# Optimization experiments

Hardware: AMD Instinct MI355X
Metric: run time of the kernel (lower is better)

Reference implementation:

```python
import jax, jax.numpy as jnp
import numpy as np

B, D, U = 64, 256, 256

def setup_inputs() -> dict:
    key = jax.random.key(0)
    ks = jax.random.split(key, 16)
    init_mu = 0.05
    inputs = jax.random.normal(ks[0], (B, D), jnp.float32)
    prev_state = 0.1 * jax.random.normal(ks[1], (B, U), jnp.float32)
    A = jax.random.normal(ks[2], (B, U, U), jnp.float32)
    # symmetric, diagonally boosted covariance-like state
    Sigma_state = 0.01 * (A + jnp.swapaxes(A, 1, 2)) + 0.1 * jnp.eye(U, dtype=jnp.float32)
    def w(k, shape):
        return init_mu * jax.random.normal(k, shape, jnp.float32)
    def s(k):
        return jax.random.uniform(k, (U,), jnp.float32, -4.5, -2.2)
    return {
        'inputs': inputs, 'prev_state': prev_state, 'Sigma_state': Sigma_state,
        'U_z': w(ks[3], (D, U)), 'uz_sigma': s(ks[4]), 'W_z': w(ks[5], (U, U)), 'wz_sigma': s(ks[6]),
        'U_r': w(ks[7], (D, U)), 'ur_sigma': s(ks[8]), 'W_r': w(ks[9], (U, U)), 'wr_sigma': s(ks[10]),
        'U_h': w(ks[11], (D, U)), 'uh_sigma': s(ks[12]), 'W_h': w(ks[13], (U, U)), 'wh_sigma': s(ks[14]),
    }

def _outer(a, b):  # [B,u],[B,u] -> [B,u,u]
    return a[:, :, None] * b[:, None, :]

def _quad(W, S):  # W^T @ S @ W, S is [B,u,u]
    return jnp.matmul(jnp.matmul(W.T, S), W)

def _x_sigma_w(x, sv):  # ||x||^2 * diag(softplus sigma)
    return jnp.sum(x * x, axis=1)[:, None, None] * jnp.diag(sv)

def _tr_sigma_w(S, sv):  # trace(S) * diag(softplus sigma)
    return jnp.trace(S, axis1=1, axis2=2)[:, None, None] * jnp.diag(sv)

def _hadamard_sigma(S1, S2, m1, m2):
    # S1*S2 + diag(m1) S2 diag(m1) + diag(m2) S1 diag(m2) as elementwise/broadcast
    return S1 * S2 + _outer(m1, m1) * S2 + _outer(m2, m2) * S1

def reference(inputs, prev_state, Sigma_state, U_z, uz_sigma, W_z, wz_sigma,
              U_r, ur_sigma, W_r, wr_sigma, U_h, uh_sigma, W_h, wh_sigma):
    sp = jax.nn.softplus
    # --- z gate ---
    az = inputs @ U_z + prev_state @ W_z
    z = jax.nn.sigmoid(az)
    gz = z * (1.0 - z)  # d sigmoid
    Sz = (_quad(W_z, Sigma_state) + _x_sigma_w(prev_state, sp(wz_sigma))
          + _tr_sigma_w(Sigma_state, sp(wz_sigma)) + _x_sigma_w(inputs, sp(uz_sigma)))
    Sigma_out_z = Sz * _outer(gz, gz)
    # --- r gate ---
    ar = inputs @ U_r + prev_state @ W_r
    r = jax.nn.sigmoid(ar)
    gr = r * (1.0 - r)
    Sr = (_quad(W_r, Sigma_state) + _x_sigma_w(prev_state, sp(wr_sigma))
          + _tr_sigma_w(Sigma_state, sp(wr_sigma)) + _x_sigma_w(inputs, sp(ur_sigma)))
    Sigma_out_r = Sr * _outer(gr, gr)
    # --- h candidate ---
    g_in = prev_state * r
    ah = inputs @ U_h + g_in @ W_h
    h = jnp.tanh(ah)
    gh = 1.0 - h * h  # d tanh
    sigma_g = _hadamard_sigma(Sigma_state, Sigma_out_r, prev_state, r)
    Sh = (_quad(W_h, sigma_g) + _x_sigma_w(g_in, sp(wh_sigma))
          + _tr_sigma_w(sigma_g, sp(wh_sigma)) + _x_sigma_w(inputs, sp(uh_sigma)))
    Sigma_out_h = Sh * _outer(gh, gh)
    # --- output combination ---
    mu_out = z * prev_state + (1.0 - z) * h
    sigma_a = _hadamard_sigma(Sigma_out_z, Sigma_state, z, prev_state)
    sigma_b = _hadamard_sigma(Sigma_out_z, Sigma_out_h, 1.0 - z, h)
    Sigma_out = (sigma_a + sigma_b
                 - Sigma_out_z * _outer(prev_state, h)
                 - Sigma_out_z * _outer(h, prev_state))
    Sigma_out = jnp.where(jnp.isnan(Sigma_out) | jnp.isinf(Sigma_out),
                          jnp.zeros_like(Sigma_out), Sigma_out)
    eye = jnp.eye(Sigma_out.shape[-1], dtype=Sigma_out.dtype)
    d = jnp.abs(jnp.diagonal(Sigma_out, axis1=1, axis2=2))
    Sigma_out = Sigma_out * (1.0 - eye) + d[:, :, None] * eye
    return mu_out, Sigma_out
```

## Files before the change

kernel.cpp:

```cpp
#include <hip/hip_runtime.h>
#include <math.h>

#define UDIM 256
#define BATCH 64
#define MATN 65536
#define PITCH 280

typedef __bf16 bf16x8 __attribute__((ext_vector_type(8)));
typedef float  f32x4  __attribute__((ext_vector_type(4)));

__device__ __forceinline__ float softplusf(float x) { return log1pf(expf(x)); }
__device__ __forceinline__ float sigmoidf_(float x) { return 1.f/(1.f+expf(-x)); }

__device__ __forceinline__ bf16x8 frag_load(const __bf16* base, int rt, int kt, int lane) {
  return *(const bf16x8*)(base + (((size_t)(rt*8 + kt))*64 + lane)*8);
}

__device__ __forceinline__ bf16x8 cvt8(const float* p) {
  const float4 f0 = *(const float4*)p;
  const float4 f1 = *(const float4*)(p + 4);
  bf16x8 v;
  v[0]=(__bf16)f0.x; v[1]=(__bf16)f0.y; v[2]=(__bf16)f0.z; v[3]=(__bf16)f0.w;
  v[4]=(__bf16)f1.x; v[5]=(__bf16)f1.y; v[6]=(__bf16)f1.z; v[7]=(__bf16)f1.w;
  return v;
}

__global__ __launch_bounds__(256) void prep6(
    const float* __restrict__ Uz, const float* __restrict__ Wz,
    const float* __restrict__ Ur, const float* __restrict__ Wr,
    const float* __restrict__ Uh, const float* __restrict__ Wh,
    __bf16* __restrict__ Fu_z, __bf16* __restrict__ Fw_z,
    __bf16* __restrict__ Fu_r, __bf16* __restrict__ Fw_r,
    __bf16* __restrict__ Fu_h, __bf16* __restrict__ Fw_h,
    const float* __restrict__ S, const float* __restrict__ x,
    const float* __restrict__ prev, float* __restrict__ scal)
{
  const int t = threadIdx.x;
  if (blockIdx.z == 6) {
    const int blk = blockIdx.y*4 + blockIdx.x;
    const int b = blk*4 + (t >> 6), l = t & 63;
    const float4 xv = *(const float4*)(x + b*UDIM + l*4);
    float s0 = xv.x*xv.x + xv.y*xv.y + xv.z*xv.z + xv.w*xv.w;
    const float4 pv = *(const float4*)(prev + b*UDIM + l*4);
    float s1 = pv.x*pv.x + pv.y*pv.y + pv.z*pv.z + pv.w*pv.w;
    float s2 = 0.f;
#pragma unroll
    for (int e = 0; e < 4; ++e)
      s2 += S[(size_t)b*MATN + (size_t)(l*4 + e)*257];
    for (int off = 32; off; off >>= 1) {
      s0 += __shfl_down(s0, off);
      s1 += __shfl_down(s1, off);
      s2 += __shfl_down(s2, off);
    }
    if (l == 0) {
      atomicAdd(&scal[b], s0);
      atomicAdd(&scal[64 + b], s1);
      atomicAdd(&scal[128 + b], s2);
    }
    return;
  }
  const float* W; __bf16* F;
  switch (blockIdx.z) {
    case 0: W = Uz; F = Fu_z; break;  case 1: W = Wz; F = Fw_z; break;
    case 2: W = Ur; F = Fu_r; break;  case 3: W = Wr; F = Fw_r; break;
    case 4: W = Uh; F = Fu_h; break;  default: W = Wh; F = Fw_h; break;
  }
  const int k0 = blockIdx.y*64, n0 = blockIdx.x*64;
  __shared__ float tile[64][65];
  const int tx = t & 15, ty = t >> 4;
#pragma unroll
  for (int rr = 0; rr < 4; ++rr) {
    const int row = ty*4 + rr;
    const float4 f = *(const float4*)(W + (size_t)(k0 + row)*UDIM + n0 + tx*4);
    tile[row][tx*4+0] = f.x; tile[row][tx*4+1] = f.y;
    tile[row][tx*4+2] = f.z; tile[row][tx*4+3] = f.w;
  }
  __syncthreads();
#pragma unroll
  for (int ss = 0; ss < 2; ++ss) {
    const int s = t + ss*256;
    const int rt_l = s >> 7, kt_l = (s >> 6) & 1, lane = s & 63;
    const int nl = rt_l*16 + (lane & 15), kb = kt_l*32 + (lane >> 4)*8;
    __align__(16) __bf16 tmp[8];
#pragma unroll
    for (int e = 0; e < 8; ++e) tmp[e] = (__bf16)tile[kb + e][nl];
    *(uint4*)(F + (((size_t)((((n0 >> 4) + rt_l)*8) + (k0 >> 5) + kt_l))*64 + lane)*8)
        = *(const uint4*)tmp;
  }
}

__global__ __launch_bounds__(256) void sconvf(
    const float* __restrict__ S, __bf16* __restrict__ Sf)
{
  const int bx = blockIdx.x, by = blockIdx.y, b = blockIdx.z;
  const size_t sb = (size_t)b * MATN;
  const int t = threadIdx.x;
#pragma unroll
  for (int ss = 0; ss < 2; ++ss) {
    const int s = t + ss*256;
    const int chunk = s >> 6, lane = s & 63;
    const int rt_l = chunk >> 1, kt_l = chunk & 1;
    const int row = by*64 + rt_l*16 + (lane & 15);
    const int col = bx*64 + kt_l*32 + (lane >> 4)*8;
    const bf16x8 v = cvt8(S + sb + (size_t)row*UDIM + col);
    *(bf16x8*)(Sf + sb + (((size_t)((by*4 + rt_l)*8 + bx*2 + kt_l))*64 + lane)*8) = v;
  }
}

__global__ __launch_bounds__(256) void gates_zr(
    const float* __restrict__ x, const float* __restrict__ prev,
    const __bf16* __restrict__ Fu_z, const __bf16* __restrict__ Fw_z,
    const __bf16* __restrict__ Fu_r, const __bf16* __restrict__ Fw_r,
    float* __restrict__ zb, float* __restrict__ rb,
    float* __restrict__ gzb, float* __restrict__ grb,
    float* __restrict__ gin, float* __restrict__ scal)
{
  const int jt = blockIdx.x;
  const int gate = blockIdx.y;
  const __bf16* FU = gate ? Fu_r : Fu_z;
  const __bf16* FW = gate ? Fw_r : Fw_z;
  const int t = threadIdx.x, w = t >> 6, l = t & 63, r = l & 15, q = l >> 4;
  const int mrow = w*16 + r;

  f32x4 acc[4] = {};
#pragma unroll
  for (int ks = 0; ks < 16; ++ks) {
    const int k0 = ks*32;
    const float* asrc; const __bf16* B; int kk;
    if (k0 < 256) { asrc = x    + (size_t)mrow*UDIM + k0         + q*8; B = FU; kk = k0; }
    else          { asrc = prev + (size_t)mrow*UDIM + (k0 - 256) + q*8; B = FW; kk = k0 - 256; }
    const bf16x8 af = cvt8(asrc);
#pragma unroll
    for (int ni = 0; ni < 4; ++ni) {
      const bf16x8 bv = frag_load(B, jt*4 + ni, kk >> 5, l);
      acc[ni] = __builtin_amdgcn_mfma_f32_16x16x32_bf16(af, bv, acc[ni], 0, 0, 0);
    }
  }

  if (gate == 0) {
#pragma unroll
    for (int ni = 0; ni < 4; ++ni) {
      const int n = jt*64 + ni*16 + r;
#pragma unroll
      for (int v = 0; v < 4; ++v) {
        const int m = w*16 + q*4 + v;
        const float zv = sigmoidf_(acc[ni][v]);
        zb[m*UDIM + n]  = zv;
        gzb[m*UDIM + n] = zv * (1.f - zv);
      }
    }
  } else {
    float ggp[4] = {0.f, 0.f, 0.f, 0.f};
#pragma unroll
    for (int ni = 0; ni < 4; ++ni) {
      const int n = jt*64 + ni*16 + r;
#pragma unroll
      for (int v = 0; v < 4; ++v) {
        const int m = w*16 + q*4 + v;
        const float rv = sigmoidf_(acc[ni][v]);
        const float pv = prev[m*UDIM + n];
        const float g2 = pv * rv;
        rb[m*UDIM + n]  = rv;
        grb[m*UDIM + n] = rv * (1.f - rv);
        gin[m*UDIM + n] = g2;
        ggp[v] += g2 * g2;
      }
    }
#pragma unroll
    for (int s = 1; s < 16; s <<= 1)
#pragma unroll
      for (int v = 0; v < 4; ++v) ggp[v] += __shfl_xor(ggp[v], s);
    if (r == 0)
#pragma unroll
      for (int v = 0; v < 4; ++v)
        atomicAdd(&scal[192 + w*16 + q*4 + v], ggp[v]);
  }
}

__global__ __launch_bounds__(256) void gates_h(
    const float* __restrict__ x, const float* __restrict__ gin,
    const __bf16* __restrict__ Fu_h, const __bf16* __restrict__ Fw_h,
    const float* __restrict__ prev, const float* __restrict__ zb,
    float* __restrict__ hb, float* __restrict__ ghb, float* __restrict__ mu_out)
{
  const int jt = blockIdx.x;
  const int t = threadIdx.x, w = t >> 6, l = t & 63, r = l & 15, q = l >> 4;
  const int mrow = w*16 + r;

  f32x4 acc[4] = {};
#pragma unroll
  for (int ks = 0; ks < 16; ++ks) {
    const int k0 = ks*32;
    const float* asrc; const __bf16* B; int kk;
    if (k0 < 256) { asrc = x   + (size_t)mrow*UDIM + k0         + q*8; B = Fu_h; kk = k0; }
    else          { asrc = gin + (size_t)mrow*UDIM + (k0 - 256) + q*8; B = Fw_h; kk = k0 - 256; }
    const bf16x8 af = cvt8(asrc);
#pragma unroll
    for (int ni = 0; ni < 4; ++ni) {
      const bf16x8 bv = frag_load(B, jt*4 + ni, kk >> 5, l);
      acc[ni] = __builtin_amdgcn_mfma_f32_16x16x32_bf16(af, bv, acc[ni], 0, 0, 0);
    }
  }
#pragma unroll
  for (int ni = 0; ni < 4; ++ni) {
    const int n = jt*64 + ni*16 + r;
#pragma unroll
    for (int v = 0; v < 4; ++v) {
      const int m = w*16 + q*4 + v;
      const float hv = tanhf(acc[ni][v]);
      const float zv = zb[m*UDIM + n];
      hb[m*UDIM + n]  = hv;
      ghb[m*UDIM + n] = 1.f - hv*hv;
      mu_out[m*UDIM + n] = zv * prev[m*UDIM + n] + (1.f - zv) * hv;
    }
  }
}

__global__ __launch_bounds__(256, 4) void quad_zr(
    const float* __restrict__ S, const __bf16* __restrict__ Sf,
    const float* __restrict__ prev,
    const float* __restrict__ rb, const float* __restrict__ gzb,
    const float* __restrict__ grb,
    const float* __restrict__ wz_s, const float* __restrict__ uz_s,
    const float* __restrict__ wr_s, const float* __restrict__ ur_s,
    const __bf16* __restrict__ Fw_z, const __bf16* __restrict__ Fw_r,
    float* __restrict__ scal, __bf16* __restrict__ Szb, __bf16* __restrict__ G)
{
  const int bid = blockIdx.x;
  const int s = bid >> 6, b = bid & 63;
  const size_t sb = (size_t)b * MATN;
  const int t = threadIdx.x, w = t >> 6, l = t & 63, r = l & 15, q = l >> 4;
  const __bf16* Sfb = Sf + sb;

  __shared__ __align__(16) __bf16 Tz[16*PITCH];
  __shared__ __align__(16) __bf16 Tr[16*PITCH];

  f32x4 az[4] = {}, ar[4] = {};
#pragma unroll
  for (int kt = 0; kt < 8; ++kt) {
    const bf16x8 afz = frag_load(Fw_z, s, kt, l);
    const bf16x8 afr = frag_load(Fw_r, s, kt, l);
#pragma unroll
    for (int ct = 0; ct < 4; ++ct) {
      const bf16x8 bv = frag_load(Sfb, w*4 + ct, kt, l);
      az[ct] = __builtin_amdgcn_mfma_f32_16x16x32_bf16(afz, bv, az[ct], 0, 0, 0);
      ar[ct] = __builtin_amdgcn_mfma_f32_16x16x32_bf16(afr, bv, ar[ct], 0, 0, 0);
    }
  }
#pragma unroll
  for (int ct = 0; ct < 4; ++ct)
#pragma unroll
    for (int v = 0; v < 4; ++v) {
      const int row = q*4 + v, col = w*64 + ct*16 + r;
      Tz[row*PITCH + col] = (__bf16)az[ct][v];
      Tr[row*PITCH + col] = (__bf16)ar[ct][v];
    }
  __syncthreads();

  f32x4 qz[4] = {}, qr[4] = {};
#pragma unroll
  for (int kt = 0; kt < 8; ++kt) {
    const bf16x8 atz = *(const bf16x8*)&Tz[r*PITCH + kt*32 + q*8];
    const bf16x8 atr = *(const bf16x8*)&Tr[r*PITCH + kt*32 + q*8];
#pragma unroll
    for (int ct = 0; ct < 4; ++ct) {
      const bf16x8 bz = frag_load(Fw_z, w*4 + ct, kt, l);
      const bf16x8 br = frag_load(Fw_r, w*4 + ct, kt, l);
      qz[ct] = __builtin_amdgcn_mfma_f32_16x16x32_bf16(atz, bz, qz[ct], 0, 0, 0);
      qr[ct] = __builtin_amdgcn_mfma_f32_16x16x32_bf16(atr, br, qr[ct], 0, 0, 0);
    }
  }

  const float xx = scal[b];
  const float dscal = scal[64 + b] + scal[128 + b];
  const int ib = s*16 + q*4;

  {
    const f32x4 g4 = *(const f32x4*)(gzb + b*UDIM + ib);
    __align__(16) __bf16 o16[16];
#pragma unroll
    for (int ct = 0; ct < 4; ++ct) {
      const int j = (w*4 + ct)*16 + r;
      const float gj = gzb[b*UDIM + j];
#pragma unroll
      for (int v = 0; v < 4; ++v) {
        const int i = ib + v;
        float qv = qz[ct][v];
        if (i == j) qv += dscal*softplusf(wz_s[i]) + xx*softplusf(uz_s[i]);
        o16[ct*4 + v] = (__bf16)(qv * g4[v] * gj);
      }
    }
    __bf16* dst = Szb + ((size_t)(b*16 + s)*256 + t)*16;
    *(uint4*)dst       = *(const uint4*)&o16[0];
    *(uint4*)(dst + 8) = *(const uint4*)&o16[8];
  }

  float gvals[16];
  float trg = 0.f;
  {
    const f32x4 g4 = *(const f32x4*)(grb + b*UDIM + ib);
    const f32x4 p4 = *(const f32x4*)(prev + b*UDIM + ib);
    const f32x4 r4 = *(const f32x4*)(rb + b*UDIM + ib);
#pragma unroll
    for (int ct = 0; ct < 4; ++ct) {
      const int j = (w*4 + ct)*16 + r;
      const float gj = grb[b*UDIM + j];
      const float pj = prev[b*UDIM + j];
      const float rj = rb[b*UDIM + j];
#pragma unroll
      for (int v = 0; v < 4; ++v) {
        const int i = ib + v;
        float qv = qr[ct][v];
        if (i == j) qv += dscal*softplusf(wr_s[i]) + xx*softplusf(ur_s[i]);
        const float Sg = qv * g4[v] * gj;
        const float sv = S[sb + (size_t)i*UDIM + j];
        const float go = Sg*(sv + p4[v]*pj) + r4[v]*rj*sv;
        gvals[ct*4 + v] = go;
        if (i == j) trg += go;
      }
    }
  }
  if (trg != 0.f) atomicAdd(&scal[256 + b], trg);

  __syncthreads();
#pragma unroll
  for (int ct = 0; ct < 4; ++ct)
#pragma unroll
    for (int v = 0; v < 4; ++v)
      Tz[(q*4 + v)*PITCH + w*64 + ct*16 + r] = (__bf16)gvals[ct*4 + v];
  __syncthreads();
#pragma unroll
  for (int ee = 0; ee < 2; ++ee) {
    const int e = t + ee*256;
    const int kt = e >> 6, le = e & 63;
    const uint4 vv = *(const uint4*)&Tz[(le & 15)*PITCH + kt*32 + (le >> 4)*8];
    *(uint4*)(G + sb + (((size_t)(s*8 + kt))*64 + le)*8) = vv;
  }
}

__global__ __launch_bounds__(256, 4) void quad_h(
    const float* __restrict__ S, const __bf16* __restrict__ Szb,
    const float* __restrict__ prev, const float* __restrict__ zb,
    const float* __restrict__ hb, const float* __restrict__ ghb,
    const float* __restrict__ wh_s, const float* __restrict__ uh_s,
    const __bf16* __restrict__ Fw_h, const __bf16* __restrict__ G,
    const float* __restrict__ scal, float* __restrict__ out_sig)
{
  const int bid = blockIdx.x;
  const int s = bid >> 6, b = bid & 63;
  const size_t sb = (size_t)b * MATN;
  const int t = threadIdx.x, w = t >> 6, l = t & 63, r = l & 15, q = l >> 4;
  const __bf16* Gb = G + sb;

  __shared__ __align__(16) __bf16 Th[16*PITCH];

  f32x4 ah[4] = {};
#pragma unroll
  for (int kt = 0; kt < 8; ++kt) {
    const bf16x8 af = frag_load(Fw_h, s, kt, l);
#pragma unroll
    for (int ct = 0; ct < 4; ++ct) {
      const bf16x8 bv = frag_load(Gb, w*4 + ct, kt, l);
      ah[ct] = __builtin_amdgcn_mfma_f32_16x16x32_bf16(af, bv, ah[ct], 0, 0, 0);
    }
  }
#pragma unroll
  for (int ct = 0; ct < 4; ++ct)
#pragma unroll
    for (int v = 0; v < 4; ++v)
      Th[(q*4 + v)*PITCH + w*64 + ct*16 + r] = (__bf16)ah[ct][v];
  __syncthreads();

  f32x4 qh[4] = {};
#pragma unroll
  for (int kt = 0; kt < 8; ++kt) {
    const bf16x8 at = *(const bf16x8*)&Th[r*PITCH + kt*32 + q*8];
#pragma unroll
    for (int ct = 0; ct < 4; ++ct) {
      const bf16x8 bv = frag_load(Fw_h, w*4 + ct, kt, l);
      qh[ct] = __builtin_amdgcn_mfma_f32_16x16x32_bf16(at, bv, qh[ct], 0, 0, 0);
    }
  }

  const float xx = scal[b];
  const float dscal = scal[192 + b] + scal[256 + b];
  const int ib = s*16 + q*4;

  const __bf16* szp = Szb + ((size_t)(b*16 + s)*256 + t)*16;
  __align__(16) __bf16 sz16[16];
  *(uint4*)&sz16[0] = *(const uint4*)szp;
  *(uint4*)&sz16[8] = *(const uint4*)(szp + 8);

  const f32x4 g4 = *(const f32x4*)(ghb + b*UDIM + ib);
  const f32x4 p4 = *(const f32x4*)(prev + b*UDIM + ib);
  const f32x4 z4 = *(const f32x4*)(zb + b*UDIM + ib);
  const f32x4 h4 = *(const f32x4*)(hb + b*UDIM + ib);

#pragma unroll
  for (int ct = 0; ct < 4; ++ct) {
    const int j = (w*4 + ct)*16 + r;
    const float gj = ghb[b*UDIM + j];
    const float pj = prev[b*UDIM + j];
    const float zj = zb[b*UDIM + j];
    const float hj = hb[b*UDIM + j];
#pragma unroll
    for (int v = 0; v < 4; ++v) {
      const int i = ib + v;
      float qv = qh[ct][v];
      if (i == j) qv += dscal*softplusf(wh_s[i]) + xx*softplusf(uh_s[i]);
      const float Sg = qv * g4[v] * gj;
      const float sv = S[sb + (size_t)i*UDIM + j];
      const float sz = (float)sz16[ct*4 + v];
      float val = sv*(sz + z4[v]*zj)
                + sz*(p4[v] - h4[v])*(pj - hj)
                + Sg*(sz + (1.f - z4[v])*(1.f - zj));
      if (!isfinite(val)) val = 0.f;
      if (i == j) val = fabsf(val);
      out_sig[sb + (size_t)i*UDIM + j] = val;
    }
  }
}

extern "C" void kernel_launch(void* const* d_in, const int* in_sizes, int n_in,
                              void* d_out, int out_size, void* d_ws, size_t ws_size,
                              hipStream_t stream) {
  const float* x    = (const float*)d_in[0];
  const float* prev = (const float*)d_in[1];
  const float* S    = (const float*)d_in[2];
  const float* Uz   = (const float*)d_in[3];
  const float* uz_s = (const float*)d_in[4];
  const float* Wz   = (const float*)d_in[5];
  const float* wz_s = (const float*)d_in[6];
  const float* Ur   = (const float*)d_in[7];
  const float* ur_s = (const float*)d_in[8];
  const float* Wr   = (const float*)d_in[9];
  const float* wr_s = (const float*)d_in[10];
  const float* Uh   = (const float*)d_in[11];
  const float* uh_s = (const float*)d_in[12];
  const float* Wh   = (const float*)d_in[13];
  const float* wh_s = (const float*)d_in[14];

  float* out_mu  = (float*)d_out;
  float* out_sig = out_mu + BATCH*UDIM;

  float* ws   = (float*)d_ws;
  float* zb   = ws;
  float* rb   = zb  + BATCH*UDIM;
  float* gzb  = rb  + BATCH*UDIM;
  float* grb  = gzb + BATCH*UDIM;
  float* gin  = grb + BATCH*UDIM;
  float* hb   = gin + BATCH*UDIM;
  float* ghb  = hb  + BATCH*UDIM;
  float* scal = ghb + BATCH*UDIM;
  __bf16* bws  = (__bf16*)(scal + 512);
  __bf16* Fu_z = bws;
  __bf16* Fw_z = Fu_z + MATN;
  __bf16* Fu_r = Fw_z + MATN;
  __bf16* Fw_r = Fu_r + MATN;
  __bf16* Fu_h = Fw_r + MATN;
  __bf16* Fw_h = Fu_h + MATN;
  const size_t BIG = (size_t)BATCH * MATN;
  __bf16* Szb = Fw_h + MATN;
  __bf16* G   = Szb + BIG;
  __bf16* Sf  = G + BIG;

  hipMemsetAsync(scal, 0, 512*sizeof(float), stream);

  prep6<<<dim3(4,4,7), 256, 0, stream>>>(Uz, Wz, Ur, Wr, Uh, Wh,
      Fu_z, Fw_z, Fu_r, Fw_r, Fu_h, Fw_h, S, x, prev, scal);
  sconvf<<<dim3(4,4,64), 256, 0, stream>>>(S, Sf);
  gates_zr<<<dim3(4,2), 256, 0, stream>>>(x, prev, Fu_z, Fw_z, Fu_r, Fw_r,
      zb, rb, gzb, grb, gin, scal);
  gates_h<<<dim3(4), 256, 0, stream>>>(x, gin, Fu_h, Fw_h, prev, zb,
      hb, ghb, out_mu);
  quad_zr<<<dim3(1024), 256, 0, stream>>>(S, Sf, prev, rb, gzb, grb,
      wz_s, uz_s, wr_s, ur_s, Fw_z, Fw_r, scal, Szb, G);
  quad_h<<<dim3(1024), 256, 0, stream>>>(S, Szb, prev, zb, hb, ghb,
      wh_s, uh_s, Fw_h, G, scal, out_sig);
}
```

Measured before the change: 176.6 us.

## Merge prep kernels, precompute bf16 S in epilogue layout, fold gates_h into quad_zr

```diff
diff --git a/kernel.cpp b/kernel.cpp
--- a/kernel.cpp
+++ b/kernel.cpp
@@ -25,85 +25,113 @@
   return v;
 }
 
-__global__ __launch_bounds__(256) void prep6(
+__global__ __launch_bounds__(256) void prepk(
+    const float* __restrict__ S, const float* __restrict__ x,
+    const float* __restrict__ prev,
     const float* __restrict__ Uz, const float* __restrict__ Wz,
     const float* __restrict__ Ur, const float* __restrict__ Wr,
     const float* __restrict__ Uh, const float* __restrict__ Wh,
     __bf16* __restrict__ Fu_z, __bf16* __restrict__ Fw_z,
     __bf16* __restrict__ Fu_r, __bf16* __restrict__ Fw_r,
     __bf16* __restrict__ Fu_h, __bf16* __restrict__ Fw_h,
-    const float* __restrict__ S, const float* __restrict__ x,
-    const float* __restrict__ prev, float* __restrict__ scal)
+    __bf16* __restrict__ Sf, __bf16* __restrict__ Sc,
+    float* __restrict__ scal)
 {
+  __shared__ float tile[64][65];
+  const int u = blockIdx.x;
   const int t = threadIdx.x;
-  if (blockIdx.z == 6) {
-    const int blk = blockIdx.y*4 + blockIdx.x;
-    const int b = blk*4 + (t >> 6), l = t & 63;
-    const float4 xv = *(const float4*)(x + b*UDIM + l*4);
-    float s0 = xv.x*xv.x + xv.y*xv.y + xv.z*xv.z + xv.w*xv.w;
-    const float4 pv = *(const float4*)(prev + b*UDIM + l*4);
-    float s1 = pv.x*pv.x + pv.y*pv.y + pv.z*pv.z + pv.w*pv.w;
-    float s2 = 0.f;
-#pragma unroll
-    for (int e = 0; e < 4; ++e)
-      s2 += S[(size_t)b*MATN + (size_t)(l*4 + e)*257];
-    for (int off = 32; off; off >>= 1) {
-      s0 += __shfl_down(s0, off);
-      s1 += __shfl_down(s1, off);
-      s2 += __shfl_down(s2, off);
-    }
-    if (l == 0) {
-      atomicAdd(&scal[b], s0);
-      atomicAdd(&scal[64 + b], s1);
-      atomicAdd(&scal[128 + b], s2);
+
+  if (u < 1024) {
+    const int bx = u & 3, by = (u >> 2) & 3, b = u >> 4;
+    const size_t sb = (size_t)b * MATN;
+    const int tx = t & 15, ty = t >> 4;
+#pragma unroll
+    for (int rr = 0; rr < 4; ++rr) {
+      const int row = ty*4 + rr;
+      const float4 f = *(const float4*)(S + sb + (size_t)(by*64 + row)*UDIM + bx*64 + tx*4);
+      tile[row][tx*4+0] = f.x; tile[row][tx*4+1] = f.y;
+      tile[row][tx*4+2] = f.z; tile[row][tx*4+3] = f.w;
+    }
+    __syncthreads();
+#pragma unroll
+    for (int ss = 0; ss < 2; ++ss) {
+      const int s = t + ss*256;
+      const int chunk = s >> 6, lane = s & 63;
+      const int rt_l = chunk >> 1, kt_l = chunk & 1;
+      const int rl = rt_l*16 + (lane & 15), cl = kt_l*32 + (lane >> 4)*8;
+      __align__(16) __bf16 tmp[8];
+#pragma unroll
+      for (int e = 0; e < 8; ++e) tmp[e] = (__bf16)tile[rl][cl + e];
+      *(uint4*)(Sf + sb + (((size_t)((by*4 + rt_l)*8 + bx*2 + kt_l))*64 + lane)*8)
+          = *(const uint4*)tmp;
+    }
+    {
+      const int sl = t >> 6, le = t & 63, q = le >> 4, r = le & 15;
+      __align__(16) __bf16 c16[16];
+#pragma unroll
+      for (int ct = 0; ct < 4; ++ct)
+#pragma unroll
+        for (int v = 0; v < 4; ++v)
+          c16[ct*4 + v] = (__bf16)tile[sl*16 + q*4 + v][ct*16 + r];
+      __bf16* dst = Sc + ((size_t)(b*16 + by*4 + sl)*256 + bx*64 + le)*16;
+      *(uint4*)dst       = *(const uint4*)&c16[0];
+      *(uint4*)(dst + 8) = *(const uint4*)&c16[8];
     }
     return;
   }
-  const float* W; __bf16* F;
-  switch (blockIdx.z) {
-    case 0: W = Uz; F = Fu_z; break;  case 1: W = Wz; F = Fw_z; break;
-    case 2: W = Ur; F = Fu_r; break;  case 3: W = Wr; F = Fw_r; break;
-    case 4: W = Uh; F = Fu_h; break;  default: W = Wh; F = Fw_h; break;
-  }
-  const int k0 = blockIdx.y*64, n0 = blockIdx.x*64;
-  __shared__ float tile[64][65];
-  const int tx = t & 15, ty = t >> 4;
-#pragma unroll
-  for (int rr = 0; rr < 4; ++rr) {
-    const int row = ty*4 + rr;
-    const float4 f = *(const float4*)(W + (size_t)(k0 + row)*UDIM + n0 + tx*4);
-    tile[row][tx*4+0] = f.x; tile[row][tx*4+1] = f.y;
-    tile[row][tx*4+2] = f.z; tile[row][tx*4+3] = f.w;
-  }
-  __syncthreads();
-#pragma unroll
-  for (int ss = 0; ss < 2; ++ss) {
-    const int s = t + ss*256;
-    const int rt_l = s >> 7, kt_l = (s >> 6) & 1, lane = s & 63;
-    const int nl = rt_l*16 + (lane & 15), kb = kt_l*32 + (lane >> 4)*8;
-    __align__(16) __bf16 tmp[8];
-#pragma unroll
-    for (int e = 0; e < 8; ++e) tmp[e] = (__bf16)tile[kb + e][nl];
-    *(uint4*)(F + (((size_t)((((n0 >> 4) + rt_l)*8) + (k0 >> 5) + kt_l))*64 + lane)*8)
-        = *(const uint4*)tmp;
-  }
-}
-
-__global__ __launch_bounds__(256) void sconvf(
-    const float* __restrict__ S, __bf16* __restrict__ Sf)
-{
-  const int bx = blockIdx.x, by = blockIdx.y, b = blockIdx.z;
-  const size_t sb = (size_t)b * MATN;
-  const int t = threadIdx.x;
-#pragma unroll
-  for (int ss = 0; ss < 2; ++ss) {
-    const int s = t + ss*256;
-    const int chunk = s >> 6, lane = s & 63;
-    const int rt_l = chunk >> 1, kt_l = chunk & 1;
-    const int row = by*64 + rt_l*16 + (lane & 15);
-    const int col = bx*64 + kt_l*32 + (lane >> 4)*8;
-    const bf16x8 v = cvt8(S + sb + (size_t)row*UDIM + col);
-    *(bf16x8*)(Sf + sb + (((size_t)((by*4 + rt_l)*8 + bx*2 + kt_l))*64 + lane)*8) = v;
+
+  if (u < 1120) {
+    const int uu = u - 1024;
+    const int mat = uu >> 4, tl = uu & 15;
+    const int n0 = (tl & 3)*64, k0 = (tl >> 2)*64;
+    const float* W; __bf16* F;
+    switch (mat) {
+      case 0: W = Uz; F = Fu_z; break;  case 1: W = Wz; F = Fw_z; break;
+      case 2: W = Ur; F = Fu_r; break;  case 3: W = Wr; F = Fw_r; break;
+      case 4: W = Uh; F = Fu_h; break;  default: W = Wh; F = Fw_h; break;
+    }
+    const int tx = t & 15, ty = t >> 4;
+#pragma unroll
+    for (int rr = 0; rr < 4; ++rr) {
+      const int row = ty*4 + rr;
+      const float4 f = *(const float4*)(W + (size_t)(k0 + row)*UDIM + n0 + tx*4);
+      tile[row][tx*4+0] = f.x; tile[row][tx*4+1] = f.y;
+      tile[row][tx*4+2] = f.z; tile[row][tx*4+3] = f.w;
+    }
+    __syncthreads();
+#pragma unroll
+    for (int ss = 0; ss < 2; ++ss) {
+      const int s = t + ss*256;
+      const int rt_l = s >> 7, kt_l = (s >> 6) & 1, lane = s & 63;
+      const int nl = rt_l*16 + (lane & 15), kb = kt_l*32 + (lane >> 4)*8;
+      __align__(16) __bf16 tmp[8];
+#pragma unroll
+      for (int e = 0; e < 8; ++e) tmp[e] = (__bf16)tile[kb + e][nl];
+      *(uint4*)(F + (((size_t)((((n0 >> 4) + rt_l)*8) + (k0 >> 5) + kt_l))*64 + lane)*8)
+          = *(const uint4*)tmp;
+    }
+    return;
+  }
+
+  const int blk = u - 1120;
+  const int b = blk*4 + (t >> 6), l = t & 63;
+  const float4 xv = *(const float4*)(x + b*UDIM + l*4);
+  float s0 = xv.x*xv.x + xv.y*xv.y + xv.z*xv.z + xv.w*xv.w;
+  const float4 pv = *(const float4*)(prev + b*UDIM + l*4);
+  float s1 = pv.x*pv.x + pv.y*pv.y + pv.z*pv.z + pv.w*pv.w;
+  float s2 = 0.f;
+#pragma unroll
+  for (int e = 0; e < 4; ++e)
+    s2 += S[(size_t)b*MATN + (size_t)(l*4 + e)*257];
+  for (int off = 32; off; off >>= 1) {
+    s0 += __shfl_down(s0, off);
+    s1 += __shfl_down(s1, off);
+    s2 += __shfl_down(s2, off);
+  }
+  if (l == 0) {
+    atomicAdd(&scal[b], s0);
+    atomicAdd(&scal[64 + b], s1);
+    atomicAdd(&scal[128 + b], s2);
   }
 }
 
@@ -177,63 +205,60 @@
   }
 }
 
-__global__ __launch_bounds__(256) void gates_h(
+__global__ __launch_bounds__(256, 4) void quad_zr(
+    const __bf16* __restrict__ Sf, const __bf16* __restrict__ Sc,
     const float* __restrict__ x, const float* __restrict__ gin,
-    const __bf16* __restrict__ Fu_h, const __bf16* __restrict__ Fw_h,
-    const float* __restrict__ prev, const float* __restrict__ zb,
-    float* __restrict__ hb, float* __restrict__ ghb, float* __restrict__ mu_out)
-{
-  const int jt = blockIdx.x;
-  const int t = threadIdx.x, w = t >> 6, l = t & 63, r = l & 15, q = l >> 4;
-  const int mrow = w*16 + r;
-
-  f32x4 acc[4] = {};
-#pragma unroll
-  for (int ks = 0; ks < 16; ++ks) {
-    const int k0 = ks*32;
-    const float* asrc; const __bf16* B; int kk;
-    if (k0 < 256) { asrc = x   + (size_t)mrow*UDIM + k0         + q*8; B = Fu_h; kk = k0; }
-    else          { asrc = gin + (size_t)mrow*UDIM + (k0 - 256) + q*8; B = Fw_h; kk = k0 - 256; }
-    const bf16x8 af = cvt8(asrc);
-#pragma unroll
-    for (int ni = 0; ni < 4; ++ni) {
-      const bf16x8 bv = frag_load(B, jt*4 + ni, kk >> 5, l);
-      acc[ni] = __builtin_amdgcn_mfma_f32_16x16x32_bf16(af, bv, acc[ni], 0, 0, 0);
-    }
-  }
-#pragma unroll
-  for (int ni = 0; ni < 4; ++ni) {
-    const int n = jt*64 + ni*16 + r;
-#pragma unroll
-    for (int v = 0; v < 4; ++v) {
-      const int m = w*16 + q*4 + v;
-      const float hv = tanhf(acc[ni][v]);
-      const float zv = zb[m*UDIM + n];
-      hb[m*UDIM + n]  = hv;
-      ghb[m*UDIM + n] = 1.f - hv*hv;
-      mu_out[m*UDIM + n] = zv * prev[m*UDIM + n] + (1.f - zv) * hv;
-    }
-  }
-}
-
-__global__ __launch_bounds__(256, 4) void quad_zr(
-    const float* __restrict__ S, const __bf16* __restrict__ Sf,
-    const float* __restrict__ prev,
-    const float* __restrict__ rb, const float* __restrict__ gzb,
-    const float* __restrict__ grb,
+    const float* __restrict__ prev, const float* __restrict__ rb,
+    const float* __restrict__ zb,
+    const float* __restrict__ gzb, const float* __restrict__ grb,
     const float* __restrict__ wz_s, const float* __restrict__ uz_s,
     const float* __restrict__ wr_s, const float* __restrict__ ur_s,
     const __bf16* __restrict__ Fw_z, const __bf16* __restrict__ Fw_r,
-    float* __restrict__ scal, __bf16* __restrict__ Szb, __bf16* __restrict__ G)
+    const __bf16* __restrict__ Fu_h, const __bf16* __restrict__ Fw_h,
+    float* __restrict__ scal, __bf16* __restrict__ Szb, __bf16* __restrict__ G,
+    float* __restrict__ hb, float* __restrict__ ghb, float* __restrict__ mu_out)
 {
+  __shared__ __align__(16) __bf16 Tz[16*PITCH];
+  __shared__ __align__(16) __bf16 Tr[16*PITCH];
   const int bid = blockIdx.x;
+  const int t = threadIdx.x, w = t >> 6, l = t & 63, r = l & 15, q = l >> 4;
+
+  if (bid >= 1024) {
+    const int jt = bid - 1024;
+    const int mrow = w*16 + r;
+    f32x4 acc[4] = {};
+#pragma unroll
+    for (int ks = 0; ks < 16; ++ks) {
+      const int k0 = ks*32;
+      const float* asrc; const __bf16* B; int kk;
+      if (k0 < 256) { asrc = x   + (size_t)mrow*UDIM + k0         + q*8; B = Fu_h; kk = k0; }
+      else          { asrc = gin + (size_t)mrow*UDIM + (k0 - 256) + q*8; B = Fw_h; kk = k0 - 256; }
+      const bf16x8 af = cvt8(asrc);
+#pragma unroll
+      for (int ni = 0; ni < 4; ++ni) {
+        const bf16x8 bv = frag_load(B, jt*4 + ni, kk >> 5, l);
+        acc[ni] = __builtin_amdgcn_mfma_f32_16x16x32_bf16(af, bv, acc[ni], 0, 0, 0);
+      }
+    }
+#pragma unroll
+    for (int ni = 0; ni < 4; ++ni) {
+      const int n = jt*64 + ni*16 + r;
+#pragma unroll
+      for (int v = 0; v < 4; ++v) {
+        const int m = w*16 + q*4 + v;
+        const float hv = tanhf(acc[ni][v]);
+        const float zv = zb[m*UDIM + n];
+        hb[m*UDIM + n]  = hv;
+        ghb[m*UDIM + n] = 1.f - hv*hv;
+        mu_out[m*UDIM + n] = zv * prev[m*UDIM + n] + (1.f - zv) * hv;
+      }
+    }
+    return;
+  }
+
   const int s = bid >> 6, b = bid & 63;
   const size_t sb = (size_t)b * MATN;
-  const int t = threadIdx.x, w = t >> 6, l = t & 63, r = l & 15, q = l >> 4;
   const __bf16* Sfb = Sf + sb;
-
-  __shared__ __align__(16) __bf16 Tz[16*PITCH];
-  __shared__ __align__(16) __bf16 Tr[16*PITCH];
 
   f32x4 az[4] = {}, ar[4] = {};
 #pragma unroll
@@ -274,6 +299,11 @@
   const float xx = scal[b];
   const float dscal = scal[64 + b] + scal[128 + b];
   const int ib = s*16 + q*4;
+
+  const __bf16* scp = Sc + ((size_t)(b*16 + s)*256 + t)*16;
+  __align__(16) __bf16 sc16[16];
+  *(uint4*)&sc16[0] = *(const uint4*)scp;
+  *(uint4*)&sc16[8] = *(const uint4*)(scp + 8);
 
   {
     const f32x4 g4 = *(const f32x4*)(gzb + b*UDIM + ib);
@@ -313,7 +343,7 @@
         float qv = qr[ct][v];
         if (i == j) qv += dscal*softplusf(wr_s[i]) + xx*softplusf(ur_s[i]);
         const float Sg = qv * g4[v] * gj;
-        const float sv = S[sb + (size_t)i*UDIM + j];
+        const float sv = (float)sc16[ct*4 + v];
         const float go = Sg*(sv + p4[v]*pj) + r4[v]*rj*sv;
         gvals[ct*4 + v] = go;
         if (i == j) trg += go;
@@ -339,7 +369,7 @@
 }
 
 __global__ __launch_bounds__(256, 4) void quad_h(
-    const float* __restrict__ S, const __bf16* __restrict__ Szb,
+    const __bf16* __restrict__ Sc, const __bf16* __restrict__ Szb,
     const float* __restrict__ prev, const float* __restrict__ zb,
     const float* __restrict__ hb, const float* __restrict__ ghb,
     const float* __restrict__ wh_s, const float* __restrict__ uh_s,
@@ -391,6 +421,11 @@
   *(uint4*)&sz16[0] = *(const uint4*)szp;
   *(uint4*)&sz16[8] = *(const uint4*)(szp + 8);
 
+  const __bf16* scp = Sc + ((size_t)(b*16 + s)*256 + t)*16;
+  __align__(16) __bf16 sc16[16];
+  *(uint4*)&sc16[0] = *(const uint4*)scp;
+  *(uint4*)&sc16[8] = *(const uint4*)(scp + 8);
+
   const f32x4 g4 = *(const f32x4*)(ghb + b*UDIM + ib);
   const f32x4 p4 = *(const f32x4*)(prev + b*UDIM + ib);
   const f32x4 z4 = *(const f32x4*)(zb + b*UDIM + ib);
@@ -409,7 +444,7 @@
       float qv = qh[ct][v];
       if (i == j) qv += dscal*softplusf(wh_s[i]) + xx*softplusf(uh_s[i]);
       const float Sg = qv * g4[v] * gj;
-      const float sv = S[sb + (size_t)i*UDIM + j];
+      const float sv = (float)sc16[ct*4 + v];
       const float sz = (float)sz16[ct*4 + v];
       float val = sv*(sz + z4[v]*zj)
                 + sz*(p4[v] - h4[v])*(pj - hj)
@@ -463,18 +498,17 @@
   __bf16* Szb = Fw_h + MATN;
   __bf16* G   = Szb + BIG;
   __bf16* Sf  = G + BIG;
+  __bf16* Sc  = Sf + BIG;
 
   hipMemsetAsync(scal, 0, 512*sizeof(float), stream);
 
-  prep6<<<dim3(4,4,7), 256, 0, stream>>>(Uz, Wz, Ur, Wr, Uh, Wh,
-      Fu_z, Fw_z, Fu_r, Fw_r, Fu_h, Fw_h, S, x, prev, scal);
-  sconvf<<<dim3(4,4,64), 256, 0, stream>>>(S, Sf);
+  prepk<<<dim3(1136), 256, 0, stream>>>(S, x, prev, Uz, Wz, Ur, Wr, Uh, Wh,
+      Fu_z, Fw_z, Fu_r, Fw_r, Fu_h, Fw_h, Sf, Sc, scal);
   gates_zr<<<dim3(4,2), 256, 0, stream>>>(x, prev, Fu_z, Fw_z, Fu_r, Fw_r,
       zb, rb, gzb, grb, gin, scal);
-  gates_h<<<dim3(4), 256, 0, stream>>>(x, gin, Fu_h, Fw_h, prev, zb,
-      hb, ghb, out_mu);
-  quad_zr<<<dim3(1024), 256, 0, stream>>>(S, Sf, prev, rb, gzb, grb,
-      wz_s, uz_s, wr_s, ur_s, Fw_z, Fw_r, scal, Szb, G);
-  quad_h<<<dim3(1024), 256, 0, stream>>>(S, Szb, prev, zb, hb, ghb,
+  quad_zr<<<dim3(1028), 256, 0, stream>>>(Sf, Sc, x, gin, prev, rb, zb,
+      gzb, grb, wz_s, uz_s, wr_s, ur_s, Fw_z, Fw_r, Fu_h, Fw_h,
+      scal, Szb, G, hb, ghb, out_mu);
+  quad_h<<<dim3(1024), 256, 0, stream>>>(Sc, Szb, prev, zb, hb, ghb,
       wh_s, uh_s, Fw_h, G, scal, out_sig);
 }
```

Result: slower. 197.9 us (+12.0%).

## Merge small gate GEMM kernels into neighbouring launches to cut launch count

Applied to the files above, without the earlier changes.

```diff
diff --git a/kernel.cpp b/kernel.cpp
--- a/kernel.cpp
+++ b/kernel.cpp
@@ -25,7 +25,7 @@
   return v;
 }
 
-__global__ __launch_bounds__(256) void prep6(
+__global__ __launch_bounds__(256) void prep_w(
     const float* __restrict__ Uz, const float* __restrict__ Wz,
     const float* __restrict__ Ur, const float* __restrict__ Wr,
     const float* __restrict__ Uh, const float* __restrict__ Wh,
@@ -35,9 +35,10 @@
     const float* __restrict__ S, const float* __restrict__ x,
     const float* __restrict__ prev, float* __restrict__ scal)
 {
+  const int u = blockIdx.x;
   const int t = threadIdx.x;
-  if (blockIdx.z == 6) {
-    const int blk = blockIdx.y*4 + blockIdx.x;
+  if (u >= 96) {
+    const int blk = u - 96;
     const int b = blk*4 + (t >> 6), l = t & 63;
     const float4 xv = *(const float4*)(x + b*UDIM + l*4);
     float s0 = xv.x*xv.x + xv.y*xv.y + xv.z*xv.z + xv.w*xv.w;
@@ -59,13 +60,14 @@
     }
     return;
   }
+  const int mat = u >> 4, tl = u & 15;
+  const int n0 = (tl & 3)*64, k0 = (tl >> 2)*64;
   const float* W; __bf16* F;
-  switch (blockIdx.z) {
+  switch (mat) {
     case 0: W = Uz; F = Fu_z; break;  case 1: W = Wz; F = Fw_z; break;
     case 2: W = Ur; F = Fu_r; break;  case 3: W = Wr; F = Fw_r; break;
     case 4: W = Uh; F = Fu_h; break;  default: W = Wh; F = Fw_h; break;
   }
-  const int k0 = blockIdx.y*64, n0 = blockIdx.x*64;
   __shared__ float tile[64][65];
   const int tx = t & 15, ty = t >> 4;
 #pragma unroll
@@ -89,12 +91,81 @@
   }
 }
 
-__global__ __launch_bounds__(256) void sconvf(
-    const float* __restrict__ S, __bf16* __restrict__ Sf)
+__global__ __launch_bounds__(256) void sconv_gates(
+    const float* __restrict__ S, __bf16* __restrict__ Sf,
+    const float* __restrict__ x, const float* __restrict__ prev,
+    const __bf16* __restrict__ Fu_z, const __bf16* __restrict__ Fw_z,
+    const __bf16* __restrict__ Fu_r, const __bf16* __restrict__ Fw_r,
+    float* __restrict__ zb, float* __restrict__ rb,
+    float* __restrict__ gzb, float* __restrict__ grb,
+    float* __restrict__ gin, float* __restrict__ scal)
 {
-  const int bx = blockIdx.x, by = blockIdx.y, b = blockIdx.z;
+  const int bid = blockIdx.x;
+  const int t = threadIdx.x, w = t >> 6, l = t & 63, r = l & 15, q = l >> 4;
+
+  if (bid < 8) {
+    const int jt = bid & 3, gate = bid >> 2;
+    const __bf16* FU = gate ? Fu_r : Fu_z;
+    const __bf16* FW = gate ? Fw_r : Fw_z;
+    const int mrow = w*16 + r;
+    f32x4 acc[4] = {};
+#pragma unroll
+    for (int ks = 0; ks < 16; ++ks) {
+      const int k0 = ks*32;
+      const float* asrc; const __bf16* B; int kk;
+      if (k0 < 256) { asrc = x    + (size_t)mrow*UDIM + k0         + q*8; B = FU; kk = k0; }
+      else          { asrc = prev + (size_t)mrow*UDIM + (k0 - 256) + q*8; B = FW; kk = k0 - 256; }
+      const bf16x8 af = cvt8(asrc);
+#pragma unroll
+      for (int ni = 0; ni < 4; ++ni) {
+        const bf16x8 bv = frag_load(B, jt*4 + ni, kk >> 5, l);
+        acc[ni] = __builtin_amdgcn_mfma_f32_16x16x32_bf16(af, bv, acc[ni], 0, 0, 0);
+      }
+    }
+    if (gate == 0) {
+#pragma unroll
+      for (int ni = 0; ni < 4; ++ni) {
+        const int n = jt*64 + ni*16 + r;
+#pragma unroll
+        for (int v = 0; v < 4; ++v) {
+          const int m = w*16 + q*4 + v;
+          const float zv = sigmoidf_(acc[ni][v]);
+          zb[m*UDIM + n]  = zv;
+          gzb[m*UDIM + n] = zv * (1.f - zv);
+        }
+      }
+    } else {
+      float ggp[4] = {0.f, 0.f, 0.f, 0.f};
+#pragma unroll
+      for (int ni = 0; ni < 4; ++ni) {
+        const int n = jt*64 + ni*16 + r;
+#pragma unroll
+        for (int v = 0; v < 4; ++v) {
+          const int m = w*16 + q*4 + v;
+          const float rv = sigmoidf_(acc[ni][v]);
+          const float pv = prev[m*UDIM + n];
+          const float g2 = pv * rv;
+          rb[m*UDIM + n]  = rv;
+          grb[m*UDIM + n] = rv * (1.f - rv);
+          gin[m*UDIM + n] = g2;
+          ggp[v] += g2 * g2;
+        }
+      }
+#pragma unroll
+      for (int s = 1; s < 16; s <<= 1)
+#pragma unroll
+        for (int v = 0; v < 4; ++v) ggp[v] += __shfl_xor(ggp[v], s);
+      if (r == 0)
+#pragma unroll
+        for (int v = 0; v < 4; ++v)
+          atomicAdd(&scal[192 + w*16 + q*4 + v], ggp[v]);
+    }
+    return;
+  }
+
+  const int u = bid - 8;
+  const int bx = u & 3, by = (u >> 2) & 3, b = u >> 4;
   const size_t sb = (size_t)b * MATN;
-  const int t = threadIdx.x;
 #pragma unroll
   for (int ss = 0; ss < 2; ++ss) {
     const int s = t + ss*256;
@@ -107,116 +178,7 @@
   }
 }
 
-__global__ __launch_bounds__(256) void gates_zr(
-    const float* __restrict__ x, const float* __restrict__ prev,
-    const __bf16* __restrict__ Fu_z, const __bf16* __restrict__ Fw_z,
-    const __bf16* __restrict__ Fu_r, const __bf16* __restrict__ Fw_r,
-    float* __restrict__ zb, float* __restrict__ rb,
-    float* __restrict__ gzb, float* __restrict__ grb,
-    float* __restrict__ gin, float* __restrict__ scal)
-{
-  const int jt = blockIdx.x;
-  const int gate = blockIdx.y;
-  const __bf16* FU = gate ? Fu_r : Fu_z;
-  const __bf16* FW = gate ? Fw_r : Fw_z;
-  const int t = threadIdx.x, w = t >> 6, l = t & 63, r = l & 15, q = l >> 4;
-  const int mrow = w*16 + r;
-
-  f32x4 acc[4] = {};
-#pragma unroll
-  for (int ks = 0; ks < 16; ++ks) {
-    const int k0 = ks*32;
-    const float* asrc; const __bf16* B; int kk;
-    if (k0 < 256) { asrc = x    + (size_t)mrow*UDIM + k0         + q*8; B = FU; kk = k0; }
-    else          { asrc = prev + (size_t)mrow*UDIM + (k0 - 256) + q*8; B = FW; kk = k0 - 256; }
-    const bf16x8 af = cvt8(asrc);
-#pragma unroll
-    for (int ni = 0; ni < 4; ++ni) {
-      const bf16x8 bv = frag_load(B, jt*4 + ni, kk >> 5, l);
-      acc[ni] = __builtin_amdgcn_mfma_f32_16x16x32_bf16(af, bv, acc[ni], 0, 0, 0);
-    }
-  }
-
-  if (gate == 0) {
-#pragma unroll
-    for (int ni = 0; ni < 4; ++ni) {
-      const int n = jt*64 + ni*16 + r;
-#pragma unroll
-      for (int v = 0; v < 4; ++v) {
-        const int m = w*16 + q*4 + v;
-        const float zv = sigmoidf_(acc[ni][v]);
-        zb[m*UDIM + n]  = zv;
-        gzb[m*UDIM + n] = zv * (1.f - zv);
-      }
-    }
-  } else {
-    float ggp[4] = {0.f, 0.f, 0.f, 0.f};
-#pragma unroll
-    for (int ni = 0; ni < 4; ++ni) {
-      const int n = jt*64 + ni*16 + r;
-#pragma unroll
-      for (int v = 0; v < 4; ++v) {
-        const int m = w*16 + q*4 + v;
-        const float rv = sigmoidf_(acc[ni][v]);
-        const float pv = prev[m*UDIM + n];
-        const float g2 = pv * rv;
-        rb[m*UDIM + n]  = rv;
-        grb[m*UDIM + n] = rv * (1.f - rv);
-        gin[m*UDIM + n] = g2;
-        ggp[v] += g2 * g2;
-      }
-    }
-#pragma unroll
-    for (int s = 1; s < 16; s <<= 1)
-#pragma unroll
-      for (int v = 0; v < 4; ++v) ggp[v] += __shfl_xor(ggp[v], s);
-    if (r == 0)
-#pragma unroll
-      for (int v = 0; v < 4; ++v)
-        atomicAdd(&scal[192 + w*16 + q*4 + v], ggp[v]);
-  }
-}
-
-__global__ __launch_bounds__(256) void gates_h(
-    const float* __restrict__ x, const float* __restrict__ gin,
-    const __bf16* __restrict__ Fu_h, const __bf16* __restrict__ Fw_h,
-    const float* __restrict__ prev, const float* __restrict__ zb,
-    float* __restrict__ hb, float* __restrict__ ghb, float* __restrict__ mu_out)
-{
-  const int jt = blockIdx.x;
-  const int t = threadIdx.x, w = t >> 6, l = t & 63, r = l & 15, q = l >> 4;
-  const int mrow = w*16 + r;
-
-  f32x4 acc[4] = {};
-#pragma unroll
-  for (int ks = 0; ks < 16; ++ks) {
-    const int k0 = ks*32;
-    const float* asrc; const __bf16* B; int kk;
-    if (k0 < 256) { asrc = x   + (size_t)mrow*UDIM + k0         + q*8; B = Fu_h; kk = k0; }
-    else          { asrc = gin + (size_t)mrow*UDIM + (k0 - 256) + q*8; B = Fw_h; kk = k0 - 256; }
-    const bf16x8 af = cvt8(asrc);
-#pragma unroll
-    for (int ni = 0; ni < 4; ++ni) {
-      const bf16x8 bv = frag_load(B, jt*4 + ni, kk >> 5, l);
-      acc[ni] = __builtin_amdgcn_mfma_f32_16x16x32_bf16(af, bv, acc[ni], 0, 0, 0);
-    }
-  }
-#pragma unroll
-  for (int ni = 0; ni < 4; ++ni) {
-    const int n = jt*64 + ni*16 + r;
-#pragma unroll
-    for (int v = 0; v < 4; ++v) {
-      const int m = w*16 + q*4 + v;
-      const float hv = tanhf(acc[ni][v]);
-      const float zv = zb[m*UDIM + n];
-      hb[m*UDIM + n]  = hv;
-      ghb[m*UDIM + n] = 1.f - hv*hv;
-      mu_out[m*UDIM + n] = zv * prev[m*UDIM + n] + (1.f - zv) * hv;
-    }
-  }
-}
-
-__global__ __launch_bounds__(256, 4) void quad_zr(
+__global__ __launch_bounds__(256, 4) void quad_zr_gh(
     const float* __restrict__ S, const __bf16* __restrict__ Sf,
     const float* __restrict__ prev,
     const float* __restrict__ rb, const float* __restrict__ gzb,
@@ -224,12 +186,51 @@
     const float* __restrict__ wz_s, const float* __restrict__ uz_s,
     const float* __restrict__ wr_s, const float* __restrict__ ur_s,
     const __bf16* __restrict__ Fw_z, const __bf16* __restrict__ Fw_r,
-    float* __restrict__ scal, __bf16* __restrict__ Szb, __bf16* __restrict__ G)
+    float* __restrict__ scal, __bf16* __restrict__ Szb, __bf16* __restrict__ G,
+    const float* __restrict__ x, const float* __restrict__ gin,
+    const float* __restrict__ zb,
+    const __bf16* __restrict__ Fu_h, const __bf16* __restrict__ Fw_h,
+    float* __restrict__ hb, float* __restrict__ ghb, float* __restrict__ mu_out)
 {
   const int bid = blockIdx.x;
-  const int s = bid >> 6, b = bid & 63;
+  const int t = threadIdx.x, w = t >> 6, l = t & 63, r = l & 15, q = l >> 4;
+
+  if (bid < 4) {
+    const int jt = bid;
+    const int mrow = w*16 + r;
+    f32x4 acc[4] = {};
+#pragma unroll
+    for (int ks = 0; ks < 16; ++ks) {
+      const int k0 = ks*32;
+      const float* asrc; const __bf16* B; int kk;
+      if (k0 < 256) { asrc = x   + (size_t)mrow*UDIM + k0         + q*8; B = Fu_h; kk = k0; }
+      else          { asrc = gin + (size_t)mrow*UDIM + (k0 - 256) + q*8; B = Fw_h; kk = k0 - 256; }
+      const bf16x8 af = cvt8(asrc);
+#pragma unroll
+      for (int ni = 0; ni < 4; ++ni) {
+        const bf16x8 bv = frag_load(B, jt*4 + ni, kk >> 5, l);
+        acc[ni] = __builtin_amdgcn_mfma_f32_16x16x32_bf16(af, bv, acc[ni], 0, 0, 0);
+      }
+    }
+#pragma unroll
+    for (int ni = 0; ni < 4; ++ni) {
+      const int n = jt*64 + ni*16 + r;
+#pragma unroll
+      for (int v = 0; v < 4; ++v) {
+        const int m = w*16 + q*4 + v;
+        const float hv = tanhf(acc[ni][v]);
+        const float zv = zb[m*UDIM + n];
+        hb[m*UDIM + n]  = hv;
+        ghb[m*UDIM + n] = 1.f - hv*hv;
+        mu_out[m*UDIM + n] = zv * prev[m*UDIM + n] + (1.f - zv) * hv;
+      }
+    }
+    return;
+  }
+
+  const int id = bid - 4;
+  const int s = id >> 6, b = id & 63;
   const size_t sb = (size_t)b * MATN;
-  const int t = threadIdx.x, w = t >> 6, l = t & 63, r = l & 15, q = l >> 4;
   const __bf16* Sfb = Sf + sb;
 
   __shared__ __align__(16) __bf16 Tz[16*PITCH];
@@ -466,15 +467,13 @@
 
   hipMemsetAsync(scal, 0, 512*sizeof(float), stream);
 
-  prep6<<<dim3(4,4,7), 256, 0, stream>>>(Uz, Wz, Ur, Wr, Uh, Wh,
+  prep_w<<<dim3(112), 256, 0, stream>>>(Uz, Wz, Ur, Wr, Uh, Wh,
       Fu_z, Fw_z, Fu_r, Fw_r, Fu_h, Fw_h, S, x, prev, scal);
-  sconvf<<<dim3(4,4,64), 256, 0, stream>>>(S, Sf);
-  gates_zr<<<dim3(4,2), 256, 0, stream>>>(x, prev, Fu_z, Fw_z, Fu_r, Fw_r,
-      zb, rb, gzb, grb, gin, scal);
-  gates_h<<<dim3(4), 256, 0, stream>>>(x, gin, Fu_h, Fw_h, prev, zb,
-      hb, ghb, out_mu);
-  quad_zr<<<dim3(1024), 256, 0, stream>>>(S, Sf, prev, rb, gzb, grb,
-      wz_s, uz_s, wr_s, ur_s, Fw_z, Fw_r, scal, Szb, G);
+  sconv_gates<<<dim3(1032), 256, 0, stream>>>(S, Sf, x, prev,
+      Fu_z, Fw_z, Fu_r, Fw_r, zb, rb, gzb, grb, gin, scal);
+  quad_zr_gh<<<dim3(1028), 256, 0, stream>>>(S, Sf, prev, rb, gzb, grb,
+      wz_s, uz_s, wr_s, ur_s, Fw_z, Fw_r, scal, Szb, G,
+      x, gin, zb, Fu_h, Fw_h, hb, ghb, out_mu);
   quad_h<<<dim3(1024), 256, 0, stream>>>(S, Szb, prev, zb, hb, ghb,
       wh_s, uh_s, Fw_h, G, scal, out_sig);
 }
```

Result: faster. 171.2 us (-3.1%).
